# Kernel optimization log

Hardware: AMD Instinct MI355X
Metric: run time of the kernel (lower is better)

The kernel has to match this reference:

```python
import jax, jax.numpy as jnp
import numpy as np

B, S, D = 1, 2048, 1024
NH, NKV, WS = 8, 2, 64
HD = D // NH  # 128
E, HDIM, TOPK = 16, 512, 2
FP16_MIN = -65504.0
EPS = 1e-6
AUX_COEFF = 1e-5


def rmsnorm(x, w):
    return x * jax.lax.rsqrt(jnp.mean(x * x, axis=-1, keepdims=True) + EPS) * w


def setup_inputs() -> dict:
    key = jax.random.key(0)
    ks = jax.random.split(key, 24)
    r = lambda k, shape, fan: jax.random.normal(k, shape, dtype=jnp.float32) * (1.0 / np.sqrt(fan))
    return {
        "x": jax.random.normal(ks[0], (B, S, D), dtype=jnp.float32),
        "norm1_w": jnp.ones((D,), jnp.float32),
        "wq": r(ks[1], (D, NH * HD), D), "bq": jnp.zeros((NH * HD,), jnp.float32),
        "wk": r(ks[2], (D, NKV * HD), D), "bk": jnp.zeros((NKV * HD,), jnp.float32),
        "wv": r(ks[3], (D, NKV * HD), D), "bv": jnp.zeros((NKV * HD,), jnp.float32),
        "wo": r(ks[4], (NH * HD, D), NH * HD), "bo": jnp.zeros((D,), jnp.float32),
        "sink_bias": jnp.zeros((), jnp.float32),
        "norm2_w": jnp.ones((D,), jnp.float32),
        "router_w": r(ks[5], (D, E), D), "router_b": jnp.zeros((E,), jnp.float32),
        "w1": r(ks[6], (E, D, HDIM), D), "b1": jnp.zeros((E, HDIM), jnp.float32),
        "w2": r(ks[7], (E, HDIM, D), HDIM), "b2": jnp.zeros((E, D), jnp.float32),
    }


def reference(x, norm1_w, wq, bq, wk, bk, wv, bv, wo, bo, sink_bias,
              norm2_w, router_w, router_b, w1, b1, w2, b2):
    # ---- sliding-window attention with sink softmax ----
    h = rmsnorm(x, norm1_w)
    q = (h @ wq + bq).reshape(B, S, NH, HD).transpose(0, 2, 1, 3)    # [B,NH,S,HD]
    k = (h @ wk + bk).reshape(B, S, NKV, HD).transpose(0, 2, 1, 3)   # [B,NKV,S,HD]
    v = (h @ wv + bv).reshape(B, S, NKV, HD).transpose(0, 2, 1, 3)
    k = jnp.repeat(k, NH // NKV, axis=1)  # GQA expand -> [B,NH,S,HD]
    v = jnp.repeat(v, NH // NKV, axis=1)
    scores = jnp.einsum('bhqd,bhkd->bhqk', q, k) / np.sqrt(HD)
    i = jnp.arange(S)[:, None]
    j = jnp.arange(S)[None, :]
    band = (i - j >= 0) & (i - j <= WS - 1)  # causal sliding window
    scores = jnp.where(band, scores, FP16_MIN)
    m = jnp.maximum(jnp.max(scores, axis=-1, keepdims=True), sink_bias)
    ew = jnp.exp(scores - m)
    denom = jnp.sum(ew, axis=-1, keepdims=True) + jnp.exp(sink_bias - m)
    attn = ew / denom
    out = jnp.einsum('bhqk,bhkd->bhqd', attn, v).transpose(0, 2, 1, 3).reshape(B, S, D)
    x = x + (out @ wo + bo)

    # ---- MoE FFN ----
    h2 = rmsnorm(x, norm2_w)
    xf = h2.reshape(-1, D)                                  # [N,D]
    logits = (xf @ router_w + router_b) / 0.1               # [N,E]
    top_v, top_i = jax.lax.top_k(logits, TOPK)              # [N,k]
    top_w = jax.nn.softmax(top_v, axis=-1)
    probs = jax.nn.softmax(logits, axis=-1)
    aux_loss = jnp.sum(jnp.sum(probs, axis=0) ** 2) / E * AUX_COEFF
    # combine weights per (token, expert)
    gate = jnp.sum(jax.nn.one_hot(top_i, E, dtype=xf.dtype) * top_w[..., None], axis=1)  # [N,E]
    hmid = jax.nn.silu(jnp.einsum('nd,edh->neh', xf, w1) + b1)   # [N,E,H]
    y = jnp.einsum('neh,ehd->ned', hmid, w2) + b2                # [N,E,D]
    ffn = jnp.einsum('ne,ned->nd', gate, y)
    x = x + ffn.reshape(B, S, D)
    return x, aux_loss
```

## Files before the change

kernel.cpp:

```cpp
#include <hip/hip_runtime.h>
#include <hip/hip_bf16.h>

#define S     2048
#define D     1024
#define NH    8
#define NKV   2
#define HD    128
#define WS_   64
#define E_    16
#define HDIM  512
#define TOPK  2
#define NTOK  S
#define NSLOT (S*TOPK)
#define QKV_M (D + 2*NKV*HD)
#define KOFF  D
#define VOFF  (D + NKV*HD)
#define QB    8
#define WROWS (QB + WS_ - 1)
#define KPITCH 73
#define VPADF  132
#define NTILES 80

typedef __attribute__((ext_vector_type(8))) short bf16x8;
typedef __attribute__((ext_vector_type(4))) float floatx4;

__device__ inline short f2bf(float f) {
    __hip_bfloat16 b = __float2bfloat16(f);
    return *reinterpret_cast<short*>(&b);
}

__global__ __launch_bounds__(256) void tconv_all(
    const float* __restrict__ wq, const float* __restrict__ wk,
    const float* __restrict__ wv, const float* __restrict__ wo,
    const float* __restrict__ w1, const float* __restrict__ w2,
    const float* __restrict__ bq, const float* __restrict__ bk,
    const float* __restrict__ bv, const float* __restrict__ router_w,
    short* __restrict__ wqkvT, short* __restrict__ woT,
    short* __restrict__ w1T, short* __restrict__ w2T,
    float* __restrict__ bqkv, float* __restrict__ rwT,
    const float* __restrict__ x, const float* __restrict__ norm1_w,
    short* __restrict__ h_bf)
{
    int id = blockIdx.x;
    if (id >= 18982) {
        int row = id - 18982, t = threadIdx.x;
        float4 v = ((const float4*)(x + (size_t)row * D))[t];
        float ss = v.x*v.x + v.y*v.y + v.z*v.z + v.w*v.w;
        #pragma unroll
        for (int off = 32; off; off >>= 1) ss += __shfl_xor(ss, off, 64);
        __shared__ float red[4];
        if ((t & 63) == 0) red[t >> 6] = ss;
        __syncthreads();
        float total = red[0] + red[1] + red[2] + red[3];
        float scale = rsqrtf(total * (1.0f / (float)D) + 1e-6f);
        float4 wv4 = ((const float4*)norm1_w)[t];
        short4 ob;
        ob.x = f2bf(v.x * scale * wv4.x); ob.y = f2bf(v.y * scale * wv4.y);
        ob.z = f2bf(v.z * scale * wv4.z); ob.w = f2bf(v.w * scale * wv4.w);
        ((short4*)(h_bf + (size_t)row * D))[t] = ob;
        return;
    }
    if (id >= 18950) {
        int ky = id - 18950;
        int t = threadIdx.x;
        int r = t >> 4, c = t & 15;
        int k0 = ky * 32;
        rwT[c * D + k0 + r]      = router_w[(k0 + r) * E_ + c];
        rwT[c * D + k0 + r + 16] = router_w[(k0 + r + 16) * E_ + c];
        return;
    }
    if (id >= 18944) {
        int t = (id - 18944) * 256 + threadIdx.x;
        if (t < D) bqkv[t] = bq[t];
        else if (t < VOFF) bqkv[t] = bk[t - D];
        else bqkv[t] = bv[t - VOFF];
        return;
    }
    const float* in; short* outp; int K, M, mx, ky;
    if (id < 1024)      { in = wq; outp = wqkvT;                  K = D; M = D;   int l = id;        mx = l & 31; ky = l >> 5; }
    else if (id < 1280) { in = wk; outp = wqkvT + (size_t)KOFF*D; K = D; M = 256; int l = id - 1024; mx = l & 7;  ky = l >> 3; }
    else if (id < 1536) { in = wv; outp = wqkvT + (size_t)VOFF*D; K = D; M = 256; int l = id - 1280; mx = l & 7;  ky = l >> 3; }
    else if (id < 2560) { in = wo; outp = woT;                    K = D; M = D;   int l = id - 1536; mx = l & 31; ky = l >> 5; }
    else if (id < 10752){ int l = id - 2560;  int e = l >> 9; int r = l & 511;
                          in = w1 + (size_t)e * D * HDIM; outp = w1T + (size_t)e * D * HDIM;
                          K = D; M = HDIM; mx = r & 15; ky = r >> 4; }
    else                { int l = id - 10752; int e = l >> 9; int r = l & 511;
                          in = w2 + (size_t)e * D * HDIM; outp = w2T + (size_t)e * D * HDIM;
                          K = HDIM; M = D; mx = r & 31; ky = r >> 5; }
    __shared__ float tile[32][33];
    int t = threadIdx.x, r = t >> 3, c4 = (t & 7) * 4;
    int k0 = ky * 32, m0 = mx * 32;
    float4 v = *(const float4*)&in[(size_t)(k0 + r) * M + m0 + c4];
    tile[r][c4 + 0] = v.x; tile[r][c4 + 1] = v.y;
    tile[r][c4 + 2] = v.z; tile[r][c4 + 3] = v.w;
    __syncthreads();
    short4 o;
    o.x = f2bf(tile[c4 + 0][r]);
    o.y = f2bf(tile[c4 + 1][r]);
    o.z = f2bf(tile[c4 + 2][r]);
    o.w = f2bf(tile[c4 + 3][r]);
    *(short4*)&outp[(size_t)(m0 + r) * K + k0 + c4] = o;
}

#define BT   64
#define BKS  64
#define BUFS (BT * BKS)

__device__ inline void gld16(const short* g, short* l) {
    __builtin_amdgcn_global_load_lds(
        (const __attribute__((address_space(1))) unsigned int*)g,
        (__attribute__((address_space(3))) unsigned int*)l, 16, 0, 0);
}

template <int V>
__global__ __launch_bounds__(256) void mgemm(
    const short* __restrict__ A, const short* __restrict__ Bt,
    const float* __restrict__ bias, float* __restrict__ C,
    short* __restrict__ Cb, const float* __restrict__ res, int K, int M,
    const int* __restrict__ offs, const float* __restrict__ tok_gate,
    const int* __restrict__ tok_map, const int* __restrict__ tmap)
{
    int e, row_lo, row_hi;
    if (V >= 2) {
        int y = blockIdx.y;
        if (y >= tmap[NTILES]) return;
        int tm = tmap[y];
        e      = tm >> 16;
        row_lo = tm & 0xFFFF;
        row_hi = offs[e + 1];
        if (row_lo >= row_hi) return;
    } else {
        e = 0;
        row_lo = blockIdx.y * BT;
        row_hi = 1 << 30;
    }
    const short* Bte = (V >= 2) ? Bt + (size_t)e * M * K : Bt;
    const float* be  = (V >= 2) ? bias + (size_t)e * M : bias;
    int col0 = blockIdx.x * BT;

    __shared__ __align__(16) short As[3 * BUFS];
    __shared__ __align__(16) short Bs[3 * BUFS];

    int t = threadIdx.x;
    int wave = t >> 6, lane = t & 63;
    int lrow   = lane >> 3;
    int schunk = (lane & 7) ^ lrow;

    const short* aQ[2];
    const short* bQ[2];
    #pragma unroll
    for (int q = 0; q < 2; ++q) {
        int row = q * 32 + wave * 8 + lrow;
        int gr = row_lo + row;
        if (V >= 2 && gr >= row_hi) gr = row_lo;
        const short* arow;
        if (V == 2) arow = A + (size_t)(tok_map[gr] & (NTOK - 1)) * K;
        else        arow = A + (size_t)gr * K;
        aQ[q] = arow + (schunk << 3);
        bQ[q] = Bte + (size_t)(col0 + row) * K + (schunk << 3);
    }

    int rin = lane & 15, quad = lane >> 4;
    int wm = (wave & 1) * 32, wn = (wave >> 1) * 32;

    int cg0 = col0 + wn + rin;
    int cg1 = cg0 + 16;
    float bj[2] = { be[cg0], be[cg1] };
    float resv[2][2][4];
    if (V == 1) {
        #pragma unroll
        for (int i = 0; i < 2; ++i)
            #pragma unroll
            for (int j = 0; j < 2; ++j)
                #pragma unroll
                for (int rr = 0; rr < 4; ++rr)
                    resv[i][j][rr] = res[(size_t)(row_lo + wm + i*16 + quad*4 + rr) * M
                                         + (j ? cg1 : cg0)];
    }
    int   tmv[2][4];
    float tgv[2][4];
    if (V == 3) {
        #pragma unroll
        for (int i = 0; i < 2; ++i)
            #pragma unroll
            for (int rr = 0; rr < 4; ++rr) {
                int rg = row_lo + wm + i*16 + quad*4 + rr;
                tmv[i][rr] = tok_map[rg] & (NTOK - 1);
                tgv[i][rr] = tok_gate[rg];
            }
    }

    floatx4 acc[2][2];
    #pragma unroll
    for (int i = 0; i < 2; ++i)
        #pragma unroll
        for (int j = 0; j < 2; ++j)
            acc[i][j] = (floatx4){0.f, 0.f, 0.f, 0.f};

    const int NIT = K >> 6;

    #pragma unroll
    for (int q = 0; q < 2; ++q) {
        gld16(aQ[q], &As[(q * 32 + wave * 8) * BKS]);
        gld16(bQ[q], &Bs[(q * 32 + wave * 8) * BKS]);
    }
    if (NIT > 1) {
        #pragma unroll
        for (int q = 0; q < 2; ++q) {
            gld16(aQ[q] + 64, &As[BUFS + (q * 32 + wave * 8) * BKS]);
            gld16(bQ[q] + 64, &Bs[BUFS + (q * 32 + wave * 8) * BKS]);
        }
        asm volatile("s_waitcnt vmcnt(4)\n\ts_barrier" ::: "memory");
    } else {
        asm volatile("s_waitcnt vmcnt(0)\n\ts_barrier" ::: "memory");
    }
    __builtin_amdgcn_sched_barrier(0);

    int bread = 0;
    for (int it = 0; it < NIT; ++it) {
        if (it + 2 < NIT) {
            int bst = bread + 2; if (bst >= 3) bst -= 3;
            int kk = (it + 2) << 6;
            #pragma unroll
            for (int q = 0; q < 2; ++q) {
                gld16(aQ[q] + kk, &As[bst * BUFS + (q * 32 + wave * 8) * BKS]);
                gld16(bQ[q] + kk, &Bs[bst * BUFS + (q * 32 + wave * 8) * BKS]);
            }
        }
        const short* Ab = &As[bread * BUFS];
        const short* Bb = &Bs[bread * BUFS];
        #pragma unroll
        for (int s = 0; s < 2; ++s) {
            bf16x8 af[2], bfr[2];
            #pragma unroll
            for (int i = 0; i < 2; ++i) {
                int row = wm + i * 16 + rin;
                af[i] = *(const bf16x8*)&Ab[row * BKS
                        + ((((s << 2) | quad) ^ (rin & 7)) << 3)];
            }
            #pragma unroll
            for (int j = 0; j < 2; ++j) {
                int row = wn + j * 16 + rin;
                bfr[j] = *(const bf16x8*)&Bb[row * BKS
                        + ((((s << 2) | quad) ^ (rin & 7)) << 3)];
            }
            #pragma unroll
            for (int i = 0; i < 2; ++i)
                #pragma unroll
                for (int j = 0; j < 2; ++j)
                    acc[i][j] = __builtin_amdgcn_mfma_f32_16x16x32_bf16(
                        af[i], bfr[j], acc[i][j], 0, 0, 0);
        }
        if (it + 1 < NIT) {
            if (it + 2 < NIT)
                asm volatile("s_waitcnt vmcnt(4)\n\ts_barrier" ::: "memory");
            else
                asm volatile("s_waitcnt vmcnt(0)\n\ts_barrier" ::: "memory");
            __builtin_amdgcn_sched_barrier(0);
        }
        bread = bread + 1; if (bread >= 3) bread = 0;
    }

    #pragma unroll
    for (int i = 0; i < 2; ++i) {
        #pragma unroll
        for (int j = 0; j < 2; ++j) {
            int cg = j ? cg1 : cg0;
            #pragma unroll
            for (int rr = 0; rr < 4; ++rr) {
                int rg = row_lo + wm + i * 16 + quad * 4 + rr;
                float val = acc[i][j][rr];
                if (V == 0) {
                    C[(size_t)rg * M + cg] = val + bj[j];
                } else if (V == 1) {
                    C[(size_t)rg * M + cg] = val + bj[j] + resv[i][j][rr];
                } else if (V == 2) {
                    if (rg < row_hi) {
                        float vb_ = val + bj[j];
                        Cb[(size_t)rg * M + cg] = f2bf(vb_ / (1.f + __expf(-vb_)));
                    }
                } else {
                    if (rg < row_hi)
                        unsafeAtomicAdd(&C[(size_t)tmv[i][rr] * M + cg],
                                        tgv[i][rr] * (val + bj[j]));
                }
            }
        }
    }
}

__global__ __launch_bounds__(256) void attn_kernel(
    const float* __restrict__ qkv, const float* __restrict__ sink_ptr,
    short* __restrict__ ao)
{
    __shared__ __align__(16) float KT[32 * KPITCH * 4];
    __shared__ __align__(16) float Vs[WROWS * VPADF];
    __shared__ __align__(16) float Ps4[4][64][4];

    int qblk = blockIdx.x;
    int kvh  = blockIdx.y;
    int q0   = qblk * QB;
    int jbase = q0 - (WS_ - 1);

    int t = threadIdx.x;
    int c4 = (t & 31) * 4, c4g = t & 31;
    for (int r = t >> 5; r < WROWS; r += 8) {
        int j = jbase + r;
        float4 kv4 = make_float4(0.f, 0.f, 0.f, 0.f);
        float4 vv4 = make_float4(0.f, 0.f, 0.f, 0.f);
        if (j >= 0) {
            kv4 = *(const float4*)(qkv + (size_t)j * QKV_M + KOFF + kvh * HD + c4);
            vv4 = *(const float4*)(qkv + (size_t)j * QKV_M + VOFF + kvh * HD + c4);
        }
        *(float4*)&KT[(c4g * KPITCH + r) * 4] = kv4;
        *(float4*)&Vs[r * VPADF + c4] = vv4;
    }
    __syncthreads();

    int lane = t & 63, wv = t >> 6;
    float sink = sink_ptr[0];
    const float rscale = 0.08838834764831845f;

    #pragma unroll
    for (int g = 0; g < 2; ++g) {
        int qi = wv * 2 + g;
        int i  = q0 + qi;
        bool valid = (jbase + qi + lane) >= 0;

        float sc[4] = {0.f, 0.f, 0.f, 0.f};
        const float* qbase = qkv + (size_t)i * QKV_M + (kvh * 4) * HD;
        #pragma unroll
        for (int c = 0; c < 32; ++c) {
            float4 kx = *(const float4*)&KT[(c * KPITCH + qi + lane) * 4];
            #pragma unroll
            for (int hh = 0; hh < 4; ++hh) {
                float4 q4 = *(const float4*)(qbase + hh * HD + c * 4);
                sc[hh] += q4.x*kx.x + q4.y*kx.y + q4.z*kx.z + q4.w*kx.w;
            }
        }

        float pn[4];
        #pragma unroll
        for (int hh = 0; hh < 4; ++hh) {
            float s = valid ? sc[hh] * rscale : -1e30f;
            float m = s;
            #pragma unroll
            for (int off = 32; off; off >>= 1) m = fmaxf(m, __shfl_xor(m, off, 64));
            float mf = fmaxf(m, sink);
            float p  = __expf(s - mf);
            float ds = p;
            #pragma unroll
            for (int off = 32; off; off >>= 1) ds += __shfl_xor(ds, off, 64);
            pn[hh] = p / (ds + __expf(sink - mf));
        }
        *(float4*)&Ps4[wv][lane][0] = make_float4(pn[0], pn[1], pn[2], pn[3]);

        float o0=0,o1=0,o2=0,o3=0,o4=0,o5=0,o6=0,o7=0;
        const float* vp = &Vs[qi * VPADF + 2 * lane];
        #pragma unroll
        for (int jj = 0; jj < 64; ++jj) {
            float4 p4 = *(const float4*)&Ps4[wv][jj][0];
            float2 vv = *(const float2*)(vp + jj * VPADF);
            o0 += p4.x * vv.x; o1 += p4.x * vv.y;
            o2 += p4.y * vv.x; o3 += p4.y * vv.y;
            o4 += p4.z * vv.x; o5 += p4.z * vv.y;
            o6 += p4.w * vv.x; o7 += p4.w * vv.y;
        }
        short2 r0; r0.x = f2bf(o0); r0.y = f2bf(o1);
        short2 r1; r1.x = f2bf(o2); r1.y = f2bf(o3);
        short2 r2; r2.x = f2bf(o4); r2.y = f2bf(o5);
        short2 r3; r3.x = f2bf(o6); r3.y = f2bf(o7);
        ((short2*)(ao + (size_t)i * D + (kvh * 4 + 0) * HD))[lane] = r0;
        ((short2*)(ao + (size_t)i * D + (kvh * 4 + 1) * HD))[lane] = r1;
        ((short2*)(ao + (size_t)i * D + (kvh * 4 + 2) * HD))[lane] = r2;
        ((short2*)(ao + (size_t)i * D + (kvh * 4 + 3) * HD))[lane] = r3;
    }
}

__global__ __launch_bounds__(256) void rms_router_kernel(
    const float* __restrict__ x1, const float* __restrict__ w,
    short* __restrict__ h2b, const float* __restrict__ rwT,
    const float* __restrict__ rb, float* __restrict__ probs,
    int* __restrict__ top_i, float* __restrict__ top_g,
    float* __restrict__ out)
{
    int tok = blockIdx.x, t = threadIdx.x;
    __shared__ float hrow[D];
    float4 v = ((const float4*)(x1 + (size_t)tok * D))[t];
    ((float4*)(out + (size_t)tok * D))[t] = v;
    float ss = v.x*v.x + v.y*v.y + v.z*v.z + v.w*v.w;
    #pragma unroll
    for (int off = 32; off; off >>= 1) ss += __shfl_xor(ss, off, 64);
    __shared__ float red[4];
    if ((t & 63) == 0) red[t >> 6] = ss;
    __syncthreads();
    float total = red[0] + red[1] + red[2] + red[3];
    float scale = rsqrtf(total * (1.0f / (float)D) + 1e-6f);
    float4 wv = ((const float4*)w)[t];
    float4 o;
    o.x = v.x * scale * wv.x; o.y = v.y * scale * wv.y;
    o.z = v.z * scale * wv.z; o.w = v.w * scale * wv.w;
    ((float4*)hrow)[t] = o;
    short4 ob;
    ob.x = f2bf(o.x); ob.y = f2bf(o.y); ob.z = f2bf(o.z); ob.w = f2bf(o.w);
    ((short4*)(h2b + (size_t)tok * D))[t] = ob;
    __syncthreads();

    int e = t & 15, seg = t >> 4;
    const float4* rwp = (const float4*)(rwT + (size_t)e * D + seg * 64);
    const float4* hp  = (const float4*)(hrow + seg * 64);
    float part = 0.f;
    #pragma unroll
    for (int i = 0; i < 16; ++i) {
        float4 a = hp[i];
        float4 b = rwp[i];
        part += a.x * b.x; part += a.y * b.y;
        part += a.z * b.z; part += a.w * b.w;
    }
    __shared__ float lpart[256];
    lpart[t] = part;
    __syncthreads();

    if (t < E_) {
        float sl = 0.f;
        #pragma unroll
        for (int sg = 0; sg < 16; ++sg) sl += lpart[sg * 16 + t];
        float lv = (sl + rb[t]) * 10.0f;

        float bv = lv; int bi = t;
        #pragma unroll
        for (int off = 8; off; off >>= 1) {
            float ov = __shfl_xor(bv, off, 16);
            int   oi = __shfl_xor(bi, off, 16);
            if (ov > bv || (ov == bv && oi < bi)) { bv = ov; bi = oi; }
        }
        float lv2 = (t == bi) ? -3.402823e38f : lv;
        float bv2 = lv2; int bi2 = t;
        #pragma unroll
        for (int off = 8; off; off >>= 1) {
            float ov = __shfl_xor(bv2, off, 16);
            int   oi = __shfl_xor(bi2, off, 16);
            if (ov > bv2 || (ov == bv2 && oi < bi2)) { bv2 = ov; bi2 = oi; }
        }
        float pexp = __expf(lv - bv);
        float ps = pexp;
        #pragma unroll
        for (int off = 8; off; off >>= 1) ps += __shfl_xor(ps, off, 16);
        probs[tok * E_ + t] = pexp / ps;
        if (t == 0) {
            float e1 = __expf(bv2 - bv);
            float g0 = 1.f / (1.f + e1);
            top_i[tok * 2 + 0] = bi;  top_g[tok * 2 + 0] = g0;
            top_i[tok * 2 + 1] = bi2; top_g[tok * 2 + 1] = e1 * g0;
        }
    }
}

__global__ __launch_bounds__(256) void finalize_scatter_kernel(
    const float* __restrict__ probs, const int* __restrict__ top_i,
    const float* __restrict__ top_g, int* __restrict__ offs,
    int* __restrict__ tok_idx, float* __restrict__ tok_gate,
    int* __restrict__ slot_of, float* __restrict__ aux_out,
    int* __restrict__ tmap)
{
    __shared__ float csum[E_];
    __shared__ int hist[E_];
    __shared__ int curs[E_];
    int t = threadIdx.x;
    if (t < E_) { csum[t] = 0.f; hist[t] = 0; }
    __syncthreads();

    const float4* p4 = (const float4*)probs;
    float4 a4 = make_float4(0.f, 0.f, 0.f, 0.f);
    for (int i = 0; i < (NTOK * E_ / 4) / 256; ++i) {
        float4 v = p4[i * 256 + t];
        a4.x += v.x; a4.y += v.y; a4.z += v.z; a4.w += v.w;
    }
    atomicAdd(&csum[(4 * t + 0) & 15], a4.x);
    atomicAdd(&csum[(4 * t + 1) & 15], a4.y);
    atomicAdd(&csum[(4 * t + 2) & 15], a4.z);
    atomicAdd(&csum[(4 * t + 3) & 15], a4.w);

    for (int i = 0; i < NSLOT / 256; ++i) {
        int eidx = top_i[i * 256 + t] & 15;
        atomicAdd(&hist[eidx], 1);
    }
    __syncthreads();

    if (t == 0) {
        int acc = 0, nt = 0;
        for (int e = 0; e < E_; ++e) {
            offs[e] = acc; curs[e] = acc;
            for (int rb = acc; rb < acc + hist[e]; rb += BT)
                tmap[nt++] = (e << 16) | rb;
            acc += hist[e];
        }
        offs[E_] = acc;
        tmap[NTILES] = nt;
        float s = 0.f;
        for (int e = 0; e < E_; ++e) s += csum[e] * csum[e];
        *aux_out = s / (float)E_ * 1e-5f;
    }
    __syncthreads();

    for (int i = 0; i < NTOK / 256; ++i) {
        int tok = i * 256 + t;
        #pragma unroll
        for (int s = 0; s < TOPK; ++s) {
            int e = top_i[tok * 2 + s] & 15;
            int pos = atomicAdd(&curs[e], 1) & (NSLOT - 1);
            tok_idx[pos]  = tok;
            tok_gate[pos] = top_g[tok * 2 + s];
            slot_of[tok * 2 + s] = pos;
        }
    }
}

extern "C" void kernel_launch(void* const* d_in, const int* in_sizes, int n_in,
                              void* d_out, int out_size, void* d_ws, size_t ws_size,
                              hipStream_t stream)
{
    const float* x        = (const float*)d_in[0];
    const float* norm1_w  = (const float*)d_in[1];
    const float* wq       = (const float*)d_in[2];
    const float* bq       = (const float*)d_in[3];
    const float* wk       = (const float*)d_in[4];
    const float* bk       = (const float*)d_in[5];
    const float* wv       = (const float*)d_in[6];
    const float* bv       = (const float*)d_in[7];
    const float* wo       = (const float*)d_in[8];
    const float* bo       = (const float*)d_in[9];
    const float* sink     = (const float*)d_in[10];
    const float* norm2_w  = (const float*)d_in[11];
    const float* router_w = (const float*)d_in[12];
    const float* router_b = (const float*)d_in[13];
    const float* w1       = (const float*)d_in[14];
    const float* b1       = (const float*)d_in[15];
    const float* w2       = (const float*)d_in[16];
    const float* b2       = (const float*)d_in[17];
    float* out = (float*)d_out;

    char* w = (char*)d_ws;
    auto alloc = [&](size_t bytes) {
        char* p = w; w += (bytes + 255) & ~255ull; return p;
    };
    short* wqkvT = (short*)alloc((size_t)QKV_M * D * 2);
    short* woT   = (short*)alloc((size_t)D * D * 2);
    short* w1T   = (short*)alloc((size_t)E_ * HDIM * D * 2);
    short* w2T   = (short*)alloc((size_t)E_ * D * HDIM * 2);
    float* bqkv  = (float*)alloc(QKV_M * 4);
    float* rwT   = (float*)alloc((size_t)E_ * D * 4);
    short* h_bf  = (short*)alloc((size_t)S * D * 2);
    float* qkv   = (float*)alloc((size_t)S * QKV_M * 4);
    float* x1    = (float*)alloc((size_t)S * D * 4);
    short* h2b   = (short*)alloc((size_t)S * D * 2);
    float* probs = (float*)alloc((size_t)NTOK * E_ * 4);
    int*   offs     = (int*)alloc(17 * 4);
    int*   tmap     = (int*)alloc((NTILES + 1) * 4);
    int*   top_i    = (int*)alloc((size_t)NSLOT * 4);
    float* top_g    = (float*)alloc((size_t)NSLOT * 4);
    int*   tok_idx  = (int*)alloc((size_t)NSLOT * 4);
    float* tok_gate = (float*)alloc((size_t)NSLOT * 4);
    int*   slot_of  = (int*)alloc((size_t)NSLOT * 4);
    short* ao_bf = h_bf;
    short* hmid  = (short*)qkv;

    tconv_all<<<21030, 256, 0, stream>>>(wq, wk, wv, wo, w1, w2, bq, bk, bv,
                                         router_w, wqkvT, woT, w1T, w2T,
                                         bqkv, rwT, x, norm1_w, h_bf);

    mgemm<0><<<dim3(QKV_M / BT, S / BT), 256, 0, stream>>>(
        h_bf, wqkvT, bqkv, qkv, nullptr, nullptr, D, QKV_M, nullptr, nullptr,
        nullptr, nullptr);

    attn_kernel<<<dim3(S / QB, NKV), 256, 0, stream>>>(qkv, sink, ao_bf);

    mgemm<1><<<dim3(D / BT, S / BT), 256, 0, stream>>>(
        ao_bf, woT, bo, x1, nullptr, x, D, D, nullptr, nullptr, nullptr,
        nullptr);

    rms_router_kernel<<<NTOK, 256, 0, stream>>>(x1, norm2_w, h2b, rwT,
                                                router_b, probs, top_i, top_g,
                                                out);

    finalize_scatter_kernel<<<1, 256, 0, stream>>>(
        probs, top_i, top_g, offs, tok_idx, tok_gate, slot_of,
        out + (size_t)S * D, tmap);

    mgemm<2><<<dim3(HDIM / BT, NTILES), 256, 0, stream>>>(
        h2b, w1T, b1, nullptr, hmid, nullptr, D, HDIM, offs, nullptr, tok_idx,
        tmap);

    mgemm<3><<<dim3(D / BT, NTILES), 256, 0, stream>>>(
        hmid, w2T, b2, out, nullptr, nullptr, HDIM, D, offs, tok_gate, tok_idx,
        tmap);
}
```

Measured before the change: 280.5 us.

## Scatter tokens into per-expert padded buckets in router; swizzle dense GEMM tiles

The router kernel now appends each token's two expert assignments into per-expert padded buckets using global atomic counters (padded to 32 ints apart), so the single-block finalize kernel no longer does the histogram and serial scatter loop. Finalize only reads the counts to build offsets, the tile map and the aux loss. The grouped GEMMs index tokens and gates via the expert's bucket and a local row offset. Separately, the dense GEMM variants remap block IDs with an 8-way swizzle to improve L2 locality. This adds global atomics in the router and extra zeroing work in the conversion kernel.

```diff
diff --git a/kernel.cpp b/kernel.cpp
--- a/kernel.cpp
+++ b/kernel.cpp
@@ -20,6 +20,7 @@
 #define KPITCH 73
 #define VPADF  132
 #define NTILES 80
+#define EPAD  4096
 
 typedef __attribute__((ext_vector_type(8))) short bf16x8;
 typedef __attribute__((ext_vector_type(4))) float floatx4;
@@ -39,11 +40,11 @@
     short* __restrict__ w1T, short* __restrict__ w2T,
     float* __restrict__ bqkv, float* __restrict__ rwT,
     const float* __restrict__ x, const float* __restrict__ norm1_w,
-    short* __restrict__ h_bf)
+    short* __restrict__ h_bf, int* __restrict__ ecur)
 {
     int id = blockIdx.x;
-    if (id >= 18982) {
-        int row = id - 18982, t = threadIdx.x;
+    if (id >= 18983) {
+        int row = id - 18983, t = threadIdx.x;
         float4 v = ((const float4*)(x + (size_t)row * D))[t];
         float ss = v.x*v.x + v.y*v.y + v.z*v.z + v.w*v.w;
         #pragma unroll
@@ -58,6 +59,11 @@
         ob.x = f2bf(v.x * scale * wv4.x); ob.y = f2bf(v.y * scale * wv4.y);
         ob.z = f2bf(v.z * scale * wv4.z); ob.w = f2bf(v.w * scale * wv4.w);
         ((short4*)(h_bf + (size_t)row * D))[t] = ob;
+        return;
+    }
+    if (id == 18982) {
+        int t = threadIdx.x;
+        ecur[t] = 0; ecur[t + 256] = 0;
         return;
     }
     if (id >= 18950) {
@@ -117,26 +123,32 @@
     const short* __restrict__ A, const short* __restrict__ Bt,
     const float* __restrict__ bias, float* __restrict__ C,
     short* __restrict__ Cb, const float* __restrict__ res, int K, int M,
-    const int* __restrict__ offs, const float* __restrict__ tok_gate,
-    const int* __restrict__ tok_map, const int* __restrict__ tmap)
+    const int* __restrict__ offs, const float* __restrict__ gatepad,
+    const int* __restrict__ tokpad, const int* __restrict__ tmap)
 {
-    int e, row_lo, row_hi;
+    int e, row_lo, row_hi, off_e, bx;
     if (V >= 2) {
         int y = blockIdx.y;
         if (y >= tmap[NTILES]) return;
         int tm = tmap[y];
         e      = tm >> 16;
         row_lo = tm & 0xFFFF;
+        off_e  = offs[e];
         row_hi = offs[e + 1];
         if (row_lo >= row_hi) return;
+        bx = blockIdx.x;
     } else {
-        e = 0;
-        row_lo = blockIdx.y * BT;
+        e = 0; off_e = 0;
+        int flat = blockIdx.y * gridDim.x + blockIdx.x;
+        int cpx  = (gridDim.x * gridDim.y) >> 3;
+        int swz  = (flat & 7) * cpx + (flat >> 3);
+        bx = swz % gridDim.x;
+        row_lo = (swz / gridDim.x) * BT;
         row_hi = 1 << 30;
     }
     const short* Bte = (V >= 2) ? Bt + (size_t)e * M * K : Bt;
     const float* be  = (V >= 2) ? bias + (size_t)e * M : bias;
-    int col0 = blockIdx.x * BT;
+    int col0 = bx * BT;
 
     __shared__ __align__(16) short As[3 * BUFS];
     __shared__ __align__(16) short Bs[3 * BUFS];
@@ -154,8 +166,11 @@
         int gr = row_lo + row;
         if (V >= 2 && gr >= row_hi) gr = row_lo;
         const short* arow;
-        if (V == 2) arow = A + (size_t)(tok_map[gr] & (NTOK - 1)) * K;
-        else        arow = A + (size_t)gr * K;
+        if (V == 2)
+            arow = A + (size_t)(tokpad[(e << 12) + ((gr - off_e) & (EPAD - 1))]
+                                & (NTOK - 1)) * K;
+        else
+            arow = A + (size_t)gr * K;
         aQ[q] = arow + (schunk << 3);
         bQ[q] = Bte + (size_t)(col0 + row) * K + (schunk << 3);
     }
@@ -185,8 +200,9 @@
             #pragma unroll
             for (int rr = 0; rr < 4; ++rr) {
                 int rg = row_lo + wm + i*16 + quad*4 + rr;
-                tmv[i][rr] = tok_map[rg] & (NTOK - 1);
-                tgv[i][rr] = tok_gate[rg];
+                int local = (rg - off_e) & (EPAD - 1);
+                tmv[i][rr] = tokpad[(e << 12) + local] & (NTOK - 1);
+                tgv[i][rr] = gatepad[(e << 12) + local];
             }
     }
 
@@ -381,8 +397,8 @@
     const float* __restrict__ x1, const float* __restrict__ w,
     short* __restrict__ h2b, const float* __restrict__ rwT,
     const float* __restrict__ rb, float* __restrict__ probs,
-    int* __restrict__ top_i, float* __restrict__ top_g,
-    float* __restrict__ out)
+    int* __restrict__ ecur, int* __restrict__ tokpad,
+    float* __restrict__ gatepad, float* __restrict__ out)
 {
     int tok = blockIdx.x, t = threadIdx.x;
     __shared__ float hrow[D];
@@ -450,24 +466,23 @@
         if (t == 0) {
             float e1 = __expf(bv2 - bv);
             float g0 = 1.f / (1.f + e1);
-            top_i[tok * 2 + 0] = bi;  top_g[tok * 2 + 0] = g0;
-            top_i[tok * 2 + 1] = bi2; top_g[tok * 2 + 1] = e1 * g0;
-        }
-    }
-}
-
-__global__ __launch_bounds__(256) void finalize_scatter_kernel(
-    const float* __restrict__ probs, const int* __restrict__ top_i,
-    const float* __restrict__ top_g, int* __restrict__ offs,
-    int* __restrict__ tok_idx, float* __restrict__ tok_gate,
-    int* __restrict__ slot_of, float* __restrict__ aux_out,
-    int* __restrict__ tmap)
+            float g1 = e1 * g0;
+            int p0 = atomicAdd(&ecur[bi  * 32], 1) & (EPAD - 1);
+            int p1 = atomicAdd(&ecur[bi2 * 32], 1) & (EPAD - 1);
+            tokpad[(bi  << 12) + p0] = tok;  gatepad[(bi  << 12) + p0] = g0;
+            tokpad[(bi2 << 12) + p1] = tok;  gatepad[(bi2 << 12) + p1] = g1;
+        }
+    }
+}
+
+__global__ __launch_bounds__(256) void finalize_kernel(
+    const float* __restrict__ probs, const int* __restrict__ ecur,
+    int* __restrict__ offs, int* __restrict__ tmap,
+    float* __restrict__ aux_out)
 {
     __shared__ float csum[E_];
-    __shared__ int hist[E_];
-    __shared__ int curs[E_];
     int t = threadIdx.x;
-    if (t < E_) { csum[t] = 0.f; hist[t] = 0; }
+    if (t < E_) csum[t] = 0.f;
     __syncthreads();
 
     const float4* p4 = (const float4*)probs;
@@ -480,39 +495,22 @@
     atomicAdd(&csum[(4 * t + 1) & 15], a4.y);
     atomicAdd(&csum[(4 * t + 2) & 15], a4.z);
     atomicAdd(&csum[(4 * t + 3) & 15], a4.w);
-
-    for (int i = 0; i < NSLOT / 256; ++i) {
-        int eidx = top_i[i * 256 + t] & 15;
-        atomicAdd(&hist[eidx], 1);
-    }
     __syncthreads();
 
     if (t == 0) {
         int acc = 0, nt = 0;
         for (int e = 0; e < E_; ++e) {
-            offs[e] = acc; curs[e] = acc;
-            for (int rb = acc; rb < acc + hist[e]; rb += BT)
+            int h = ecur[e * 32];
+            offs[e] = acc;
+            for (int rb = acc; rb < acc + h; rb += BT)
                 tmap[nt++] = (e << 16) | rb;
-            acc += hist[e];
+            acc += h;
         }
         offs[E_] = acc;
         tmap[NTILES] = nt;
         float s = 0.f;
         for (int e = 0; e < E_; ++e) s += csum[e] * csum[e];
         *aux_out = s / (float)E_ * 1e-5f;
-    }
-    __syncthreads();
-
-    for (int i = 0; i < NTOK / 256; ++i) {
-        int tok = i * 256 + t;
-        #pragma unroll
-        for (int s = 0; s < TOPK; ++s) {
-            int e = top_i[tok * 2 + s] & 15;
-            int pos = atomicAdd(&curs[e], 1) & (NSLOT - 1);
-            tok_idx[pos]  = tok;
-            tok_gate[pos] = top_g[tok * 2 + s];
-            slot_of[tok * 2 + s] = pos;
-        }
     }
 }
 
@@ -555,19 +553,17 @@
     float* x1    = (float*)alloc((size_t)S * D * 4);
     short* h2b   = (short*)alloc((size_t)S * D * 2);
     float* probs = (float*)alloc((size_t)NTOK * E_ * 4);
+    int*   ecur     = (int*)alloc(E_ * 32 * 4);
     int*   offs     = (int*)alloc(17 * 4);
     int*   tmap     = (int*)alloc((NTILES + 1) * 4);
-    int*   top_i    = (int*)alloc((size_t)NSLOT * 4);
-    float* top_g    = (float*)alloc((size_t)NSLOT * 4);
-    int*   tok_idx  = (int*)alloc((size_t)NSLOT * 4);
-    float* tok_gate = (float*)alloc((size_t)NSLOT * 4);
-    int*   slot_of  = (int*)alloc((size_t)NSLOT * 4);
+    int*   tokpad   = (int*)alloc((size_t)E_ * EPAD * 4);
+    float* gatepad  = (float*)alloc((size_t)E_ * EPAD * 4);
     short* ao_bf = h_bf;
     short* hmid  = (short*)qkv;
 
-    tconv_all<<<21030, 256, 0, stream>>>(wq, wk, wv, wo, w1, w2, bq, bk, bv,
+    tconv_all<<<21031, 256, 0, stream>>>(wq, wk, wv, wo, w1, w2, bq, bk, bv,
                                          router_w, wqkvT, woT, w1T, w2T,
-                                         bqkv, rwT, x, norm1_w, h_bf);
+                                         bqkv, rwT, x, norm1_w, h_bf, ecur);
 
     mgemm<0><<<dim3(QKV_M / BT, S / BT), 256, 0, stream>>>(
         h_bf, wqkvT, bqkv, qkv, nullptr, nullptr, D, QKV_M, nullptr, nullptr,
@@ -580,18 +576,17 @@
         nullptr);
 
     rms_router_kernel<<<NTOK, 256, 0, stream>>>(x1, norm2_w, h2b, rwT,
-                                                router_b, probs, top_i, top_g,
-                                                out);
-
-    finalize_scatter_kernel<<<1, 256, 0, stream>>>(
-        probs, top_i, top_g, offs, tok_idx, tok_gate, slot_of,
-        out + (size_t)S * D, tmap);
+                                                router_b, probs, ecur,
+                                                tokpad, gatepad, out);
+
+    finalize_kernel<<<1, 256, 0, stream>>>(probs, ecur, offs, tmap,
+                                           out + (size_t)S * D);
 
     mgemm<2><<<dim3(HDIM / BT, NTILES), 256, 0, stream>>>(
-        h2b, w1T, b1, nullptr, hmid, nullptr, D, HDIM, offs, nullptr, tok_idx,
+        h2b, w1T, b1, nullptr, hmid, nullptr, D, HDIM, offs, gatepad, tokpad,
         tmap);
 
     mgemm<3><<<dim3(D / BT, NTILES), 256, 0, stream>>>(
-        hmid, w2T, b2, out, nullptr, nullptr, HDIM, D, offs, tok_gate, tok_idx,
+        hmid, w2T, b2, out, nullptr, nullptr, HDIM, D, offs, gatepad, tokpad,
         tmap);
 }
```

Measured after the change: 277.1 us. Within noise of the previous version (-1.2%).
